# Optimization experiments

Measured on AMD Instinct MI355X. Metric: run time of the kernel, lower is better.

## Reference

```python
import jax, jax.numpy as jnp
import numpy as np

D = 1024

def setup_inputs() -> dict:
    key = jax.random.key(0)
    ks = jax.random.split(key, 7)
    s = 1.0 / np.sqrt(D)
    return {
        "x": jax.random.normal(ks[0], (4, 2048, D), dtype=jnp.float32),
        "Wq": jax.random.uniform(ks[1], (D, D), jnp.float32, -s, s),
        "bq": jax.random.uniform(ks[2], (D,), jnp.float32, -s, s),
        "Wk": jax.random.uniform(ks[3], (D, D), jnp.float32, -s, s),
        "bk": jax.random.uniform(ks[4], (D,), jnp.float32, -s, s),
        "Wv": jax.random.uniform(ks[5], (D, D), jnp.float32, -s, s),
        "bv": jax.random.uniform(ks[6], (D,), jnp.float32, -s, s),
    }

def reference(x, Wq, bq, Wk, bk, Wv, bv):
    # x: [B, S, D]
    q = jnp.einsum('bsd,de->bse', x, Wq.T) + bq
    k = jnp.einsum('bsd,de->bse', x, Wk.T) + bk
    v = jnp.einsum('bsd,de->bse', x, Wv.T) + bv
    scale = 1.0 / jnp.sqrt(jnp.float32(x.shape[-1]))
    score = jnp.einsum('bqd,bkd->bqk', q, k) * scale  # [B, S, S]
    attn = jax.nn.softmax(score, axis=-1)
    return jnp.einsum('bqk,bkd->bqd', attn, v)
```

## Files before the change

kernel.cpp:

```cpp
#include <hip/hip_runtime.h>

typedef short shortx8 __attribute__((ext_vector_type(8)));
typedef float floatx4 __attribute__((ext_vector_type(4)));
typedef unsigned short ushortx4 __attribute__((ext_vector_type(4)));
typedef unsigned short ushortx8 __attribute__((ext_vector_type(8)));

typedef __attribute__((address_space(1))) char gchar;
typedef __attribute__((address_space(3))) char lchar;

__device__ __forceinline__ void async16(const void* g, void* l) {
    __builtin_amdgcn_global_load_lds((gchar*)g, (lchar*)l, 16, 0, 0);
}

__device__ __forceinline__ unsigned short f2bf(float f) {
    union { float f; unsigned int u; } v;
    v.f = f;
    unsigned int r = v.u + 0x7fffu + ((v.u >> 16) & 1u);
    return (unsigned short)(r >> 16);
}

__device__ __forceinline__ float bf2f(unsigned short h) {
    union { unsigned int u; float f; } v;
    v.u = ((unsigned int)h) << 16;
    return v.f;
}

template<int JN>
__device__ __forceinline__ void gemm256_mainloop(
        const ushort* __restrict__ Arow, const ushort* __restrict__ Brow,
        int K, ushort* ldsp, floatx4 (&acc)[8][JN])
{
    const int t = threadIdx.x;
    const int w = t >> 6;
    const int lane = t & 63;
    const size_t ldb = (size_t)K * 2;
    constexpr int ABYTES = 32768;
    constexpr int BBYTES = JN * 8192;
    constexpr int BUFB = ABYTES + BBYTES;
    char* l0 = (char*)ldsp;
    const int wst = w << 10;
    const int sc = (((t & 7) ^ ((t >> 4) & 7)) << 4);
    const char* gA = (const char*)Arow + (size_t)(t >> 3) * ldb + sc;
    const char* gB = (const char*)Brow + (size_t)(t >> 3) * ldb + sc;
    const int fr = lane & 15, kq = lane >> 4;
    const int xr = (fr >> 1) & 7;
    const int ck0 = (kq ^ xr) << 4;
    const int ck1 = ((kq + 4) ^ xr) << 4;
    const int wm = w & 1, wn = w >> 1;
    const int abase = (wm * 128 + fr) * 128;
    const int bbase = (wn * (JN * 16) + fr) * 128;

#define STA(buf, kt, R) async16(gA + (size_t)(R) * ldb + (size_t)(kt) * 128, \
                                l0 + (buf) * BUFB + (R) * 128 + wst)
#define STB(buf, kt, R) async16(gB + (size_t)(R) * ldb + (size_t)(kt) * 128, \
                                l0 + (buf) * BUFB + ABYTES + (R) * 128 + wst)
#define LDA4(buf, mb, ck)                                                          \
    a0 = *(const shortx8*)(l0 + (buf) * BUFB + abase + ((mb) + 0) * 2048 + (ck));  \
    a1 = *(const shortx8*)(l0 + (buf) * BUFB + abase + ((mb) + 1) * 2048 + (ck));  \
    a2 = *(const shortx8*)(l0 + (buf) * BUFB + abase + ((mb) + 2) * 2048 + (ck));  \
    a3 = *(const shortx8*)(l0 + (buf) * BUFB + abase + ((mb) + 3) * 2048 + (ck));
#define LDBJ(buf, ck)                                                              \
    _Pragma("unroll")                                                              \
    for (int n = 0; n < JN; ++n)                                                   \
        b[n] = *(const shortx8*)(l0 + (buf) * BUFB + ABYTES + bbase + n * 2048 + (ck));
#define PHASE_MFMA(MB)                                                             \
    __builtin_amdgcn_s_setprio(1);                                                 \
    _Pragma("unroll")                                                              \
    for (int n = 0; n < JN; ++n) {                                                 \
        acc[(MB)+0][n] = __builtin_amdgcn_mfma_f32_16x16x32_bf16(a0, b[n], acc[(MB)+0][n], 0, 0, 0); \
        acc[(MB)+1][n] = __builtin_amdgcn_mfma_f32_16x16x32_bf16(a1, b[n], acc[(MB)+1][n], 0, 0, 0); \
        acc[(MB)+2][n] = __builtin_amdgcn_mfma_f32_16x16x32_bf16(a2, b[n], acc[(MB)+2][n], 0, 0, 0); \
        acc[(MB)+3][n] = __builtin_amdgcn_mfma_f32_16x16x32_bf16(a3, b[n], acc[(MB)+3][n], 0, 0, 0); \
    }                                                                              \
    __builtin_amdgcn_s_setprio(0);
#define BAR() __builtin_amdgcn_s_barrier()
#define VMW()                                              \
    asm volatile("s_waitcnt vmcnt(2)" ::: "memory");       \
    BAR();                                                 \
    __builtin_amdgcn_sched_barrier(0);

    const int nk = K >> 6;
    const int nit = nk >> 1;

    STA(0, 0, 0); STA(0, 0, 64); STA(0, 0, 128); STA(0, 0, 192);
    STB(0, 0, 0); STB(0, 0, 64);
    if (JN == 4) { STB(0, 0, 128); STB(0, 0, 192); }
    STA(1, 1, 0); STA(1, 1, 128);
    VMW();

    shortx8 a0, a1, a2, a3;
    shortx8 b[JN];

    for (int it = 0; it < nit; ++it) {
        const int T = 2 * it;
        int Tc2 = T + 2; if (Tc2 >= nk) Tc2 = T;
        int Tc3 = T + 3; if (Tc3 >= nk) Tc3 = nk - 1;

        LDA4(0, 0, ck0); LDBJ(0, ck0);
        STA(1, T + 1, 64); STA(1, T + 1, 192);
        BAR();
        PHASE_MFMA(0);
        BAR();

        LDA4(0, 4, ck0);
        STB(1, T + 1, 0);
        if (JN == 4) STB(1, T + 1, 64);
        BAR();
        PHASE_MFMA(4);
        BAR();

        LDA4(0, 0, ck1); LDBJ(0, ck1);
        if (JN == 4) { STB(1, T + 1, 128); STB(1, T + 1, 192); }
        else         { STB(1, T + 1, 64); }
        BAR();
        PHASE_MFMA(0);
        BAR();

        LDA4(0, 4, ck1);
        STA(0, Tc2, 0); STA(0, Tc2, 128);
        BAR();
        PHASE_MFMA(4);
        VMW();

        LDA4(1, 0, ck0); LDBJ(1, ck0);
        STA(0, Tc2, 64); STA(0, Tc2, 192);
        BAR();
        PHASE_MFMA(0);
        BAR();

        LDA4(1, 4, ck0);
        STB(0, Tc2, 0);
        if (JN == 4) STB(0, Tc2, 64);
        BAR();
        PHASE_MFMA(4);
        BAR();

        LDA4(1, 0, ck1); LDBJ(1, ck1);
        if (JN == 4) { STB(0, Tc2, 128); STB(0, Tc2, 192); }
        else         { STB(0, Tc2, 64); }
        BAR();
        PHASE_MFMA(0);
        BAR();

        LDA4(1, 4, ck1);
        STA(1, Tc3, 0); STA(1, Tc3, 128);
        BAR();
        PHASE_MFMA(4);
        VMW();
    }
#undef STA
#undef STB
#undef LDA4
#undef LDBJ
#undef PHASE_MFMA
#undef BAR
#undef VMW
}

__global__ __launch_bounds__(512, 2)
void qkv_gemm(const ushort* __restrict__ xb, const ushort* __restrict__ Wb,
              const float* __restrict__ bq, const float* __restrict__ bk,
              const float* __restrict__ bv,
              ushort* __restrict__ Qs, ushort* __restrict__ Ks,
              ushort* __restrict__ Vt) {
    __shared__ __align__(16) ushort lds[65536];
    const int mbase = blockIdx.y * 256;
    const int nglob = blockIdx.x * 256;
    const int z = nglob >> 10;
    const int nbase = nglob & 1023;
    floatx4 acc[8][4];
    const floatx4 zero = {0.0f, 0.0f, 0.0f, 0.0f};
#pragma unroll
    for (int i = 0; i < 8; ++i)
#pragma unroll
        for (int j = 0; j < 4; ++j) acc[i][j] = zero;

    gemm256_mainloop<4>(xb + (size_t)mbase * 1024, Wb + (size_t)nglob * 1024,
                        1024, lds, acc);

    const int t = threadIdx.x, w = t >> 6, lane = t & 63;
    const int wm = w & 1, wn = w >> 1;
    const int r0 = mbase + wm * 128 + (lane >> 4) * 4;
    const int c0 = nbase + wn * 64 + (lane & 15);
    const float* bias = (z == 0) ? bq : (z == 1) ? bk : bv;
    const float scale = (z == 0) ? 0.03125f : 1.0f;
    float bj[4];
#pragma unroll
    for (int j = 0; j < 4; ++j) bj[j] = bias[c0 + j * 16];

    if (z < 2) {
        ushort* O = z ? Ks : Qs;
#pragma unroll
        for (int i = 0; i < 8; ++i)
#pragma unroll
            for (int j = 0; j < 4; ++j)
#pragma unroll
                for (int r = 0; r < 4; ++r)
                    O[(size_t)(r0 + i * 16 + r) * 1024 + (c0 + j * 16)] =
                        f2bf((acc[i][j][r] + bj[j]) * scale);
    } else {
#pragma unroll
        for (int i = 0; i < 8; ++i)
#pragma unroll
            for (int j = 0; j < 4; ++j)
#pragma unroll
                for (int r = 0; r < 4; ++r) {
                    int gr = r0 + i * 16 + r;
                    int gc = c0 + j * 16;
                    Vt[(size_t)(gr >> 11) * (1024 * 2048) + (size_t)gc * 2048 + (gr & 2047)] =
                        f2bf(acc[i][j][r] + bj[j]);
                }
    }
}

__global__ __launch_bounds__(512, 2)
void gemm_bt_bf16(const ushort* __restrict__ A, size_t sAz,
                  const ushort* __restrict__ B, size_t sBz,
                  ushort* __restrict__ C, size_t sCz, int N, int K) {
    __shared__ __align__(16) ushort lds[65536];
    const int mbase = blockIdx.y * 256;
    const int nbase = blockIdx.x * 256;
    const int z = blockIdx.z;
    floatx4 acc[8][4];
    const floatx4 zero = {0.0f, 0.0f, 0.0f, 0.0f};
#pragma unroll
    for (int i = 0; i < 8; ++i)
#pragma unroll
        for (int j = 0; j < 4; ++j) acc[i][j] = zero;

    gemm256_mainloop<4>(A + z * sAz + (size_t)mbase * K,
                        B + z * sBz + (size_t)nbase * K, K, lds, acc);

    const int t = threadIdx.x, w = t >> 6, lane = t & 63;
    const int wm = w & 1, wn = w >> 1;
    const int r0 = mbase + wm * 128 + (lane >> 4) * 4;
    const int c0 = nbase + wn * 64 + (lane & 15);
    ushort* Cz = C + z * sCz;
#pragma unroll
    for (int i = 0; i < 8; ++i)
#pragma unroll
        for (int j = 0; j < 4; ++j)
#pragma unroll
            for (int r = 0; r < 4; ++r)
                Cz[(size_t)(r0 + i * 16 + r) * N + (c0 + j * 16)] = f2bf(acc[i][j][r]);
}

__global__ __launch_bounds__(512, 2)
void gemm_bt_f32(const ushort* __restrict__ A, size_t sAz,
                 const ushort* __restrict__ B, size_t sBz,
                 float* __restrict__ C, size_t sCz, int N, int K) {
    __shared__ __align__(16) ushort lds[49152];
    const int mbase = blockIdx.y * 256;
    const int nbase = blockIdx.x * 128;
    const int z = blockIdx.z;
    floatx4 acc[8][2];
    const floatx4 zero = {0.0f, 0.0f, 0.0f, 0.0f};
#pragma unroll
    for (int i = 0; i < 8; ++i)
#pragma unroll
        for (int j = 0; j < 2; ++j) acc[i][j] = zero;

    gemm256_mainloop<2>(A + z * sAz + (size_t)mbase * K,
                        B + z * sBz + (size_t)nbase * K, K, lds, acc);

    const int t = threadIdx.x, w = t >> 6, lane = t & 63;
    const int wm = w & 1, wn = w >> 1;
    const int r0 = mbase + wm * 128 + (lane >> 4) * 4;
    const int c0 = nbase + wn * 32 + (lane & 15);
    float* Cz = C + z * sCz;
#pragma unroll
    for (int i = 0; i < 8; ++i)
#pragma unroll
        for (int j = 0; j < 2; ++j)
#pragma unroll
            for (int r = 0; r < 4; ++r)
                Cz[(size_t)(r0 + i * 16 + r) * N + (c0 + j * 16)] = acc[i][j][r];
}

__global__ __launch_bounds__(256)
void softmax_rows_bf16(ushort* __restrict__ SP) {
    const int row = blockIdx.x;
    ushortx8* base = (ushortx8*)(SP + (size_t)row * 2048);
    const int t = threadIdx.x;
    const int w = t >> 6, lane = t & 63;
    ushortx8 v = base[t];
    float f[8];
#pragma unroll
    for (int k = 0; k < 8; ++k) f[k] = bf2f(v[k]);
    float m = f[0];
#pragma unroll
    for (int k = 1; k < 8; ++k) m = fmaxf(m, f[k]);
    for (int o = 32; o > 0; o >>= 1) m = fmaxf(m, __shfl_down(m, o));
    __shared__ float red[4];
    if (lane == 0) red[w] = m;
    __syncthreads();
    m = fmaxf(fmaxf(red[0], red[1]), fmaxf(red[2], red[3]));

    float e[8], s = 0.0f;
#pragma unroll
    for (int k = 0; k < 8; ++k) { e[k] = __expf(f[k] - m); s += e[k]; }
    for (int o = 32; o > 0; o >>= 1) s += __shfl_down(s, o);
    __syncthreads();
    if (lane == 0) red[w] = s;
    __syncthreads();
    float inv = 1.0f / (red[0] + red[1] + red[2] + red[3]);

    ushortx8 o;
#pragma unroll
    for (int k = 0; k < 8; ++k) o[k] = f2bf(e[k] * inv);
    base[t] = o;
}

__global__ __launch_bounds__(256)
void cast_bf16_all(const float* __restrict__ x, const float* __restrict__ Wq,
                   const float* __restrict__ Wk, const float* __restrict__ Wv,
                   ushort* __restrict__ dst) {
    const int NX = 2097152;
    const int NW = 262144;
    int i = blockIdx.x * 256 + threadIdx.x;
    const float* src;
    int off;
    if (i < NX)               { src = x;  off = 0; }
    else if (i < NX + NW)     { src = Wq; off = NX; }
    else if (i < NX + 2 * NW) { src = Wk; off = NX + NW; }
    else                      { src = Wv; off = NX + 2 * NW; }
    float4 v = ((const float4*)src)[i - off];
    ushortx4 o = {f2bf(v.x), f2bf(v.y), f2bf(v.z), f2bf(v.w)};
    ((ushortx4*)dst)[i] = o;
}

extern "C" void kernel_launch(void* const* d_in, const int* in_sizes, int n_in,
                              void* d_out, int out_size, void* d_ws, size_t ws_size,
                              hipStream_t stream) {
    const float* x  = (const float*)d_in[0];
    const float* bq = (const float*)d_in[2];
    const float* bk = (const float*)d_in[4];
    const float* bv = (const float*)d_in[6];
    float* out = (float*)d_out;

    const size_t R = 8192;
    const size_t D = 1024;
    const size_t S = 2048;

    const size_t need = (4 * R * D + 3 * D * D + 4 * S * S) * 2;
    if (ws_size < need) return;

    ushort* xb = (ushort*)d_ws;
    ushort* Wb = xb + R * D;
    ushort* Qs = Wb + 3 * D * D;
    ushort* Ks = Qs + R * D;
    ushort* Vt = Ks + R * D;
    ushort* Sb = Vt + R * D;

    cast_bf16_all<<<dim3(11264), dim3(256), 0, stream>>>(
        x, (const float*)d_in[1], (const float*)d_in[3], (const float*)d_in[5], xb);

    qkv_gemm<<<dim3(12, 32), dim3(512), 0, stream>>>(xb, Wb, bq, bk, bv, Qs, Ks, Vt);

    gemm_bt_bf16<<<dim3(8, 8, 4), dim3(512), 0, stream>>>(Qs, S * D, Ks, S * D, Sb, S * S,
                                                          (int)S, (int)D);

    softmax_rows_bf16<<<dim3((unsigned)(4 * S)), dim3(256), 0, stream>>>(Sb);

    gemm_bt_f32<<<dim3(8, 8, 4), dim3(512), 0, stream>>>(Sb, S * S, Vt, D * S, out, S * D,
                                                         (int)D, (int)S);
}
```

Measured before the change: 256.7 us.

## Retile QKV GEMM to 256x192 tiles and reorder mainloop with double B registers

Changes the QKV projection tile from 256x256 to 256x192, raising the grid from 384 to 512 blocks to fill the compute units more evenly. Per-column-chunk epilogue logic replaces the per-block Q/K/V selection, since a tile can now straddle the Q, K and V boundaries. The shared mainloop is rescheduled: B fragments are held in two register sets so each B load serves both A halves, the async load order is changed, and the vmcnt waits now depend on JN. This costs more registers and a less square tile in exchange for better wave balance and fewer LDS B reads.

```diff
diff --git a/kernel.cpp b/kernel.cpp
--- a/kernel.cpp
+++ b/kernel.cpp
@@ -59,102 +59,112 @@
     a1 = *(const shortx8*)(l0 + (buf) * BUFB + abase + ((mb) + 1) * 2048 + (ck));  \
     a2 = *(const shortx8*)(l0 + (buf) * BUFB + abase + ((mb) + 2) * 2048 + (ck));  \
     a3 = *(const shortx8*)(l0 + (buf) * BUFB + abase + ((mb) + 3) * 2048 + (ck));
-#define LDBJ(buf, ck)                                                              \
+#define LDB(buf, ck, dst)                                                          \
     _Pragma("unroll")                                                              \
     for (int n = 0; n < JN; ++n)                                                   \
-        b[n] = *(const shortx8*)(l0 + (buf) * BUFB + ABYTES + bbase + n * 2048 + (ck));
-#define PHASE_MFMA(MB)                                                             \
+        dst[n] = *(const shortx8*)(l0 + (buf) * BUFB + ABYTES + bbase + n * 2048 + (ck));
+#define PH(MB, BV)                                                                 \
     __builtin_amdgcn_s_setprio(1);                                                 \
     _Pragma("unroll")                                                              \
     for (int n = 0; n < JN; ++n) {                                                 \
-        acc[(MB)+0][n] = __builtin_amdgcn_mfma_f32_16x16x32_bf16(a0, b[n], acc[(MB)+0][n], 0, 0, 0); \
-        acc[(MB)+1][n] = __builtin_amdgcn_mfma_f32_16x16x32_bf16(a1, b[n], acc[(MB)+1][n], 0, 0, 0); \
-        acc[(MB)+2][n] = __builtin_amdgcn_mfma_f32_16x16x32_bf16(a2, b[n], acc[(MB)+2][n], 0, 0, 0); \
-        acc[(MB)+3][n] = __builtin_amdgcn_mfma_f32_16x16x32_bf16(a3, b[n], acc[(MB)+3][n], 0, 0, 0); \
+        acc[(MB) + 0][n] = __builtin_amdgcn_mfma_f32_16x16x32_bf16(a0, BV[n], acc[(MB) + 0][n], 0, 0, 0); \
+        acc[(MB) + 1][n] = __builtin_amdgcn_mfma_f32_16x16x32_bf16(a1, BV[n], acc[(MB) + 1][n], 0, 0, 0); \
+        acc[(MB) + 2][n] = __builtin_amdgcn_mfma_f32_16x16x32_bf16(a2, BV[n], acc[(MB) + 2][n], 0, 0, 0); \
+        acc[(MB) + 3][n] = __builtin_amdgcn_mfma_f32_16x16x32_bf16(a3, BV[n], acc[(MB) + 3][n], 0, 0, 0); \
     }                                                                              \
     __builtin_amdgcn_s_setprio(0);
 #define BAR() __builtin_amdgcn_s_barrier()
-#define VMW()                                              \
-    asm volatile("s_waitcnt vmcnt(2)" ::: "memory");       \
-    BAR();                                                 \
+#define VMW_A()                                                        \
+    asm volatile("s_waitcnt vmcnt(%0)" :: "i"(JN + 4) : "memory");     \
+    __builtin_amdgcn_s_barrier();                                      \
+    __builtin_amdgcn_sched_barrier(0);
+#define VMW_B()                                                        \
+    asm volatile("s_waitcnt vmcnt(%0)" :: "i"(JN + 2) : "memory");     \
+    __builtin_amdgcn_s_barrier();                                      \
     __builtin_amdgcn_sched_barrier(0);
 
     const int nk = K >> 6;
     const int nit = nk >> 1;
 
-    STA(0, 0, 0); STA(0, 0, 64); STA(0, 0, 128); STA(0, 0, 192);
+    STA(0, 0, 0); STA(0, 0, 128);
     STB(0, 0, 0); STB(0, 0, 64);
-    if (JN == 4) { STB(0, 0, 128); STB(0, 0, 192); }
-    STA(1, 1, 0); STA(1, 1, 128);
-    VMW();
+    if (JN >= 3) STB(0, 0, 128);
+    if (JN == 4) STB(0, 0, 192);
+    STA(0, 0, 64); STA(0, 0, 192);
+    STB(1, 1, 0); STB(1, 1, 64);
+    if (JN >= 3) STB(1, 1, 128);
+    if (JN == 4) STB(1, 1, 192);
+    asm volatile("s_waitcnt vmcnt(%0)" :: "i"(JN + 2) : "memory");
+    BAR();
+    __builtin_amdgcn_sched_barrier(0);
 
     shortx8 a0, a1, a2, a3;
-    shortx8 b[JN];
+    shortx8 b0[JN], b1[JN];
 
     for (int it = 0; it < nit; ++it) {
         const int T = 2 * it;
-        int Tc2 = T + 2; if (Tc2 >= nk) Tc2 = T;
-        int Tc3 = T + 3; if (Tc3 >= nk) Tc3 = nk - 1;
-
-        LDA4(0, 0, ck0); LDBJ(0, ck0);
-        STA(1, T + 1, 64); STA(1, T + 1, 192);
-        BAR();
-        PHASE_MFMA(0);
-        BAR();
+        const int T1 = T + 1;
+        int T2 = T + 2; if (T2 > nk - 1) T2 = nk - 1;
+        int T3 = T + 3; if (T3 > nk - 1) T3 = nk - 1;
+
+        LDA4(0, 0, ck0); LDB(0, ck0, b0);
+        STA(1, T1, 0); STA(1, T1, 128);
+        BAR();
+        PH(0, b0);
+        BAR();
+
+        LDA4(0, 0, ck1); LDB(0, ck1, b1);
+        STA(1, T1, 64); STA(1, T1, 192);
+        BAR();
+        PH(0, b1);
+        VMW_A();
 
         LDA4(0, 4, ck0);
-        STB(1, T + 1, 0);
-        if (JN == 4) STB(1, T + 1, 64);
-        BAR();
-        PHASE_MFMA(4);
-        BAR();
-
-        LDA4(0, 0, ck1); LDBJ(0, ck1);
-        if (JN == 4) { STB(1, T + 1, 128); STB(1, T + 1, 192); }
-        else         { STB(1, T + 1, 64); }
-        BAR();
-        PHASE_MFMA(0);
+        STB(0, T2, 0); STB(0, T2, 64);
+        BAR();
+        PH(4, b0);
         BAR();
 
         LDA4(0, 4, ck1);
-        STA(0, Tc2, 0); STA(0, Tc2, 128);
-        BAR();
-        PHASE_MFMA(4);
-        VMW();
-
-        LDA4(1, 0, ck0); LDBJ(1, ck0);
-        STA(0, Tc2, 64); STA(0, Tc2, 192);
-        BAR();
-        PHASE_MFMA(0);
-        BAR();
+        if (JN >= 3) STB(0, T2, 128);
+        if (JN == 4) STB(0, T2, 192);
+        BAR();
+        PH(4, b1);
+        VMW_B();
+
+        LDA4(1, 0, ck0); LDB(1, ck0, b0);
+        STA(0, T2, 0); STA(0, T2, 128);
+        BAR();
+        PH(0, b0);
+        BAR();
+
+        LDA4(1, 0, ck1); LDB(1, ck1, b1);
+        STA(0, T2, 64); STA(0, T2, 192);
+        BAR();
+        PH(0, b1);
+        VMW_A();
 
         LDA4(1, 4, ck0);
-        STB(0, Tc2, 0);
-        if (JN == 4) STB(0, Tc2, 64);
-        BAR();
-        PHASE_MFMA(4);
-        BAR();
-
-        LDA4(1, 0, ck1); LDBJ(1, ck1);
-        if (JN == 4) { STB(0, Tc2, 128); STB(0, Tc2, 192); }
-        else         { STB(0, Tc2, 64); }
-        BAR();
-        PHASE_MFMA(0);
+        STB(1, T3, 0); STB(1, T3, 64);
+        BAR();
+        PH(4, b0);
         BAR();
 
         LDA4(1, 4, ck1);
-        STA(1, Tc3, 0); STA(1, Tc3, 128);
-        BAR();
-        PHASE_MFMA(4);
-        VMW();
+        if (JN >= 3) STB(1, T3, 128);
+        if (JN == 4) STB(1, T3, 192);
+        BAR();
+        PH(4, b1);
+        VMW_B();
     }
 #undef STA
 #undef STB
 #undef LDA4
-#undef LDBJ
-#undef PHASE_MFMA
+#undef LDB
+#undef PH
 #undef BAR
-#undef VMW
+#undef VMW_A
+#undef VMW_B
 }
 
 __global__ __launch_bounds__(512, 2)
@@ -163,53 +173,52 @@
               const float* __restrict__ bv,
               ushort* __restrict__ Qs, ushort* __restrict__ Ks,
               ushort* __restrict__ Vt) {
-    __shared__ __align__(16) ushort lds[65536];
+    __shared__ __align__(16) ushort lds[57344];
     const int mbase = blockIdx.y * 256;
-    const int nglob = blockIdx.x * 256;
-    const int z = nglob >> 10;
-    const int nbase = nglob & 1023;
-    floatx4 acc[8][4];
+    const int nglob = blockIdx.x * 192;
+    floatx4 acc[8][3];
     const floatx4 zero = {0.0f, 0.0f, 0.0f, 0.0f};
 #pragma unroll
     for (int i = 0; i < 8; ++i)
 #pragma unroll
-        for (int j = 0; j < 4; ++j) acc[i][j] = zero;
-
-    gemm256_mainloop<4>(xb + (size_t)mbase * 1024, Wb + (size_t)nglob * 1024,
+        for (int j = 0; j < 3; ++j) acc[i][j] = zero;
+
+    gemm256_mainloop<3>(xb + (size_t)mbase * 1024, Wb + (size_t)nglob * 1024,
                         1024, lds, acc);
 
     const int t = threadIdx.x, w = t >> 6, lane = t & 63;
     const int wm = w & 1, wn = w >> 1;
     const int r0 = mbase + wm * 128 + (lane >> 4) * 4;
-    const int c0 = nbase + wn * 64 + (lane & 15);
-    const float* bias = (z == 0) ? bq : (z == 1) ? bk : bv;
-    const float scale = (z == 0) ? 0.03125f : 1.0f;
-    float bj[4];
-#pragma unroll
-    for (int j = 0; j < 4; ++j) bj[j] = bias[c0 + j * 16];
-
-    if (z < 2) {
-        ushort* O = z ? Ks : Qs;
-#pragma unroll
-        for (int i = 0; i < 8; ++i)
-#pragma unroll
-            for (int j = 0; j < 4; ++j)
+#pragma unroll
+    for (int j = 0; j < 3; ++j) {
+        const int cj = nglob + wn * 48 + j * 16;
+        const int z = cj >> 10;
+        const int gc = (cj & 1023) + (lane & 15);
+        const float* bias = (z == 0) ? bq : (z == 1) ? bk : bv;
+        const float bj = bias[gc];
+        if (z == 0) {
+#pragma unroll
+            for (int i = 0; i < 8; ++i)
 #pragma unroll
                 for (int r = 0; r < 4; ++r)
-                    O[(size_t)(r0 + i * 16 + r) * 1024 + (c0 + j * 16)] =
-                        f2bf((acc[i][j][r] + bj[j]) * scale);
-    } else {
-#pragma unroll
-        for (int i = 0; i < 8; ++i)
-#pragma unroll
-            for (int j = 0; j < 4; ++j)
+                    Qs[(size_t)(r0 + i * 16 + r) * 1024 + gc] =
+                        f2bf((acc[i][j][r] + bj) * 0.03125f);
+        } else if (z == 1) {
+#pragma unroll
+            for (int i = 0; i < 8; ++i)
+#pragma unroll
+                for (int r = 0; r < 4; ++r)
+                    Ks[(size_t)(r0 + i * 16 + r) * 1024 + gc] = f2bf(acc[i][j][r] + bj);
+        } else {
+#pragma unroll
+            for (int i = 0; i < 8; ++i)
 #pragma unroll
                 for (int r = 0; r < 4; ++r) {
                     int gr = r0 + i * 16 + r;
-                    int gc = c0 + j * 16;
                     Vt[(size_t)(gr >> 11) * (1024 * 2048) + (size_t)gc * 2048 + (gr & 2047)] =
-                        f2bf(acc[i][j][r] + bj[j]);
+                        f2bf(acc[i][j][r] + bj);
                 }
+        }
     }
 }
 
@@ -355,7 +364,7 @@
     cast_bf16_all<<<dim3(11264), dim3(256), 0, stream>>>(
         x, (const float*)d_in[1], (const float*)d_in[3], (const float*)d_in[5], xb);
 
-    qkv_gemm<<<dim3(12, 32), dim3(512), 0, stream>>>(xb, Wb, bq, bk, bv, Qs, Ks, Vt);
+    qkv_gemm<<<dim3(16, 32), dim3(512), 0, stream>>>(xb, Wb, bq, bk, bv, Qs, Ks, Vt);
 
     gemm_bt_bf16<<<dim3(8, 8, 4), dim3(512), 0, stream>>>(Qs, S * D, Ks, S * D, Sb, S * S,
                                                           (int)S, (int)D);
```

Result: faster. 248.8 us (-3.1%).
